# Performance work log

Measured on AMD Instinct MI355X. Metric: run time of the kernel, lower is better.

Reference implementation:

```python
import jax, jax.numpy as jnp
import numpy as np

POS_SCALE = 50.0
LEN_SCALE = 500.0

N_NODES = 100000
N_EDGES = 600000
IN_DIM = 128
HID_DIM = 128


def setup_inputs() -> dict:
    key = jax.random.key(0)
    ks = jax.random.split(key, 12)
    x = jax.random.normal(ks[0], (N_NODES, IN_DIM), dtype=jnp.float32)
    positions = jax.random.randint(ks[1], (N_NODES,), 0, 50, dtype=jnp.int64)
    lengths = jax.random.randint(ks[2], (N_NODES,), 0, 500, dtype=jnp.int64)
    edge_index = jax.random.randint(ks[3], (2, N_EDGES), 0, N_NODES, dtype=jnp.int64)
    reranker_scores = jax.random.normal(ks[4], (N_NODES,), dtype=jnp.float32)
    s = 1.0 / np.sqrt(IN_DIM + 2)
    fp_w = jax.random.uniform(ks[5], (IN_DIM + 2, IN_DIM), minval=-s, maxval=s, dtype=jnp.float32)
    fp_b = jnp.zeros((IN_DIM,), jnp.float32)
    s2 = 1.0 / np.sqrt(IN_DIM)
    lin_l_w = jax.random.uniform(ks[6], (IN_DIM, HID_DIM), minval=-s2, maxval=s2, dtype=jnp.float32)
    lin_l_b = jnp.zeros((HID_DIM,), jnp.float32)
    lin_r_w = jax.random.uniform(ks[7], (IN_DIM, HID_DIM), minval=-s2, maxval=s2, dtype=jnp.float32)
    res_w = jax.random.uniform(ks[8], (IN_DIM, HID_DIM), minval=-s2, maxval=s2, dtype=jnp.float32)
    res_b = jnp.zeros((HID_DIM,), jnp.float32)
    s3 = 1.0 / np.sqrt(HID_DIM)
    sh_w = jax.random.uniform(ks[9], (HID_DIM, 1), minval=-s3, maxval=s3, dtype=jnp.float32)
    sh_b = jnp.zeros((1,), jnp.float32)
    alpha = jnp.asarray(0.65, jnp.float32)
    return {
        "x": x, "positions": positions, "lengths": lengths,
        "edge_index": edge_index, "reranker_scores": reranker_scores,
        "fp_w": fp_w, "fp_b": fp_b,
        "lin_l_w": lin_l_w, "lin_l_b": lin_l_b, "lin_r_w": lin_r_w,
        "res_w": res_w, "res_b": res_b,
        "sh_w": sh_w, "sh_b": sh_b, "alpha": alpha,
    }


def reference(x, positions, lengths, edge_index, reranker_scores,
              fp_w, fp_b, lin_l_w, lin_l_b, lin_r_w, res_w, res_b,
              sh_w, sh_b, alpha):
    n = x.shape[0]
    # position/length features
    pos_feat = positions[:, None].astype(x.dtype) / POS_SCALE
    len_feat = lengths[:, None].astype(x.dtype) / LEN_SCALE
    xf = jnp.concatenate([x, pos_feat, len_feat], axis=-1)  # [N, D+2]
    xf = xf @ fp_w + fp_b                                   # [N, D]
    h_in = xf @ res_w + res_b                               # residual proj [N, H]
    # SAGEConv with mean aggregation: out = lin_l(mean_{j->i} x_j) + lin_r(x_i)
    src, dst = edge_index[0], edge_index[1]
    msg_sum = jax.ops.segment_sum(xf[src], dst, num_segments=n)          # [N, D]
    cnt = jax.ops.segment_sum(jnp.ones((src.shape[0], 1), xf.dtype), dst, num_segments=n)
    agg = msg_sum / jnp.maximum(cnt, 1.0)
    h = jax.nn.relu(agg @ lin_l_w + lin_l_b + xf @ lin_r_w)  # [N, H]
    # dropout is identity in eval mode
    h = h + h_in
    gnn_scores = (h @ sh_w + sh_b)[:, 0]                     # [N]
    a = jax.nn.sigmoid(alpha)
    return a * reranker_scores + (1.0 - a) * gnn_scores
```

## Files before the change

kernel.cpp:

```cpp
#include <hip/hip_runtime.h>
#include <hip/hip_bf16.h>
#include <cstdint>

#define D 128
#define LDSPITCH 136
#define CAP 32

typedef __attribute__((ext_vector_type(4))) float f32x4;
typedef __attribute__((ext_vector_type(8))) short s16x8;

__device__ __forceinline__ unsigned short f2b(float f) {
    union { float f; uint32_t u; } v; v.f = f;
    uint32_t b = v.u + 0x7fffu + ((v.u >> 16) & 1u);
    return (unsigned short)(b >> 16);
}
__device__ __forceinline__ float b2f(unsigned short u) {
    union { uint32_t u; float f; } v; v.u = ((uint32_t)u) << 16; return v.f;
}

__global__ __launch_bounds__(256) void k_prep(
    const float* __restrict__ fp_w, const float* __restrict__ lin_l_w,
    const float* __restrict__ lin_r_w,
    unsigned short* __restrict__ Btf, unsigned short* __restrict__ Btl,
    unsigned short* __restrict__ Btr,
    const float* __restrict__ res_w, const float* __restrict__ res_b,
    const float* __restrict__ sh_w, const float* __restrict__ sh_b,
    const float* __restrict__ alpha, float* __restrict__ c1, float* __restrict__ scal,
    int* __restrict__ cursor, int N) {
    int bid = blockIdx.x, tid = threadIdx.x;
    if (bid < 192) {
        int m = bid >> 6;
        int i = (bid & 63) * 256 + tid;
        const float* src = (m == 0) ? fp_w : (m == 1) ? lin_l_w : lin_r_w;
        unsigned short* dst = (m == 0) ? Btf : (m == 1) ? Btl : Btr;
        int k = i >> 7, n = i & 127;
        dst[n * D + k] = f2b(src[k * D + n]);
    } else if (bid == 192) {
        if (tid < 128) {
            float s = 0.f;
            for (int j = 0; j < D; ++j) s += res_w[tid * D + j] * sh_w[j];
            c1[tid] = s;
            if (tid == 0) {
                float c0 = 0.f;
                for (int j = 0; j < D; ++j) c0 += res_b[j] * sh_w[j];
                c0 += sh_b[0];
                float a = 1.f / (1.f + expf(-alpha[0]));
                scal[0] = a; scal[1] = c0;
            }
        }
    } else {
        int i = ((bid - 193) * 256 + tid) * 4;
        if (i < N) {
            if (i + 3 < N) *(int4*)(cursor + i) = (int4){0, 0, 0, 0};
            else { for (int k = i; k < N; ++k) cursor[k] = 0; }
        }
    }
}

__global__ __launch_bounds__(256) void k_gemm1(
    const float* __restrict__ x, unsigned short* __restrict__ xb,
    const int* __restrict__ positions, const int* __restrict__ lengths,
    const unsigned short* __restrict__ Btf,
    const float* __restrict__ fp_w, const float* __restrict__ fp_b,
    const float* __restrict__ c1, float* __restrict__ d1, int N, int mb,
    const int* __restrict__ ei, int* __restrict__ cursor, int* __restrict__ srcs, int E) {
    if (blockIdx.x >= mb) {
        int e = (blockIdx.x - mb) * 256 + threadIdx.x;
        if (e < E) {
            int src = ei[e];
            int dst = ei[E + e];
            int pos = atomicAdd(&cursor[dst], 1);
            if (pos < CAP) srcs[dst * CAP + pos] = src;
        }
        return;
    }
    int lane = threadIdx.x & 63;
    int wv = threadIdx.x >> 6;
    int col = lane & 15, q = lane >> 4;
    int row0 = blockIdx.x * 64 + wv * 16;
    int arow = row0 + col; if (arow > N - 1) arow = N - 1;

    f32x4 acc[8];
#pragma unroll
    for (int nt = 0; nt < 8; ++nt) acc[nt] = (f32x4){0.f, 0.f, 0.f, 0.f};

#pragma unroll
    for (int ks = 0; ks < 4; ++ks) {
        const float* xp = x + (size_t)arow * D + ks * 32 + q * 8;
        float4 a0 = *(const float4*)xp;
        float4 a1 = *(const float4*)(xp + 4);
        s16x8 af;
        af[0] = (short)f2b(a0.x); af[1] = (short)f2b(a0.y);
        af[2] = (short)f2b(a0.z); af[3] = (short)f2b(a0.w);
        af[4] = (short)f2b(a1.x); af[5] = (short)f2b(a1.y);
        af[6] = (short)f2b(a1.z); af[7] = (short)f2b(a1.w);
#pragma unroll
        for (int nt = 0; nt < 8; ++nt) {
            s16x8 bf = *(const s16x8*)(Btf + (size_t)(nt * 16 + col) * D + ks * 32 + q * 8);
            acc[nt] = __builtin_amdgcn_mfma_f32_16x16x32_bf16(af, bf, acc[nt], 0, 0, 0);
        }
    }

    float pf[4], lf[4];
#pragma unroll
    for (int r = 0; r < 4; ++r) {
        int rr = row0 + q * 4 + r; int rc = rr < N ? rr : N - 1;
        pf[r] = (float)positions[rc] * (1.0f / 50.0f);
        lf[r] = (float)lengths[rc] * (1.0f / 500.0f);
    }
    float sdot[4] = {0.f, 0.f, 0.f, 0.f};
#pragma unroll
    for (int nt = 0; nt < 8; ++nt) {
        int n = nt * 16 + col;
        float bias = fp_b[n];
        float w128 = fp_w[128 * D + n];
        float w129 = fp_w[129 * D + n];
        float c1v = c1[n];
#pragma unroll
        for (int r = 0; r < 4; ++r) {
            float t = acc[nt][r] + bias + pf[r] * w128 + lf[r] * w129;
            int rr = row0 + q * 4 + r;
            if (rr < N) xb[(size_t)rr * D + n] = f2b(t);
            sdot[r] += t * c1v;
        }
    }
#pragma unroll
    for (int r = 0; r < 4; ++r) {
        float s = sdot[r];
        s += __shfl_xor(s, 1, 64);
        s += __shfl_xor(s, 2, 64);
        s += __shfl_xor(s, 4, 64);
        s += __shfl_xor(s, 8, 64);
        if (col == 0) {
            int rr = row0 + q * 4 + r;
            if (rr < N) d1[rr] = s;
        }
    }
}

__global__ __launch_bounds__(256) void k_gemm2(
    const unsigned short* __restrict__ xfb,
    const int* __restrict__ cursor, const int* __restrict__ srcs,
    const unsigned short* __restrict__ Btl, const unsigned short* __restrict__ Btr,
    const float* __restrict__ lin_l_b, const float* __restrict__ sh_w,
    const float* __restrict__ rer, const float* __restrict__ d1,
    const float* __restrict__ scal, float* __restrict__ out, int N) {
    __shared__ unsigned short agg[64 * LDSPITCH];
    int lane = threadIdx.x & 63;
    int wv = threadIdx.x >> 6;
    int li = lane & 15, q = lane >> 4;
    int wrow0 = blockIdx.x * 64 + wv * 16;

#pragma unroll
    for (int rr = 0; rr < 4; ++rr) {
        int row = wrow0 + rr * 4 + q;
        float t[8] = {0.f, 0.f, 0.f, 0.f, 0.f, 0.f, 0.f, 0.f};
        int deg = 0;
        if (row < N) {
            deg = cursor[row]; if (deg > CAP) deg = CAP;
            const int* sp = srcs + (size_t)row * CAP;
            int dm1 = deg - 1;
            for (int j = 0; j < deg; j += 8) {
                int4 ia = *(const int4*)(sp + (j     < dm1 ? j     : (dm1 & ~3)));
                int4 ib;
                {
                    int jb = j + 4 <= dm1 ? j + 4 : (dm1 & ~3);
                    ib = *(const int4*)(sp + jb);
                }
                int idx[8];
                idx[0] = sp[j];
                idx[1] = j + 1 <= dm1 ? ia.y : sp[dm1];
                idx[2] = j + 2 <= dm1 ? ia.z : sp[dm1];
                idx[3] = j + 3 <= dm1 ? ia.w : sp[dm1];
                idx[4] = j + 4 <= dm1 ? ib.x : sp[dm1];
                idx[5] = j + 5 <= dm1 ? ib.y : sp[dm1];
                idx[6] = j + 6 <= dm1 ? ib.z : sp[dm1];
                idx[7] = j + 7 <= dm1 ? ib.w : sp[dm1];
                s16x8 v[8];
#pragma unroll
                for (int k = 0; k < 8; ++k)
                    v[k] = *(const s16x8*)(xfb + (size_t)idx[k] * D + li * 8);
                float w[8];
#pragma unroll
                for (int k = 0; k < 8; ++k) w[k] = (j + k < deg) ? 1.f : 0.f;
#pragma unroll
                for (int k = 0; k < 8; ++k)
#pragma unroll
                    for (int k2 = 0; k2 < 8; ++k2)
                        t[k2] += w[k] * b2f((unsigned short)v[k][k2]);
            }
        }
        float rc = 1.0f / (float)(deg > 0 ? deg : 1);
        s16x8 o;
#pragma unroll
        for (int k2 = 0; k2 < 8; ++k2) o[k2] = (short)f2b(t[k2] * rc);
        *(s16x8*)(agg + (wv * 16 + rr * 4 + q) * LDSPITCH + li * 8) = o;
    }

    int arow = wrow0 + li; if (arow > N - 1) arow = N - 1;

    f32x4 acc[8];
#pragma unroll
    for (int nt = 0; nt < 8; ++nt) acc[nt] = (f32x4){0.f, 0.f, 0.f, 0.f};

#pragma unroll
    for (int ks = 0; ks < 4; ++ks) {
        s16x8 af = *(const s16x8*)(agg + (wv * 16 + li) * LDSPITCH + ks * 32 + q * 8);
#pragma unroll
        for (int nt = 0; nt < 8; ++nt) {
            s16x8 bf = *(const s16x8*)(Btl + (size_t)(nt * 16 + li) * D + ks * 32 + q * 8);
            acc[nt] = __builtin_amdgcn_mfma_f32_16x16x32_bf16(af, bf, acc[nt], 0, 0, 0);
        }
    }
#pragma unroll
    for (int ks = 0; ks < 4; ++ks) {
        s16x8 af = *(const s16x8*)(xfb + (size_t)arow * D + ks * 32 + q * 8);
#pragma unroll
        for (int nt = 0; nt < 8; ++nt) {
            s16x8 bf = *(const s16x8*)(Btr + (size_t)(nt * 16 + li) * D + ks * 32 + q * 8);
            acc[nt] = __builtin_amdgcn_mfma_f32_16x16x32_bf16(af, bf, acc[nt], 0, 0, 0);
        }
    }

    float a = scal[0], c0 = scal[1];
    float sdot[4] = {0.f, 0.f, 0.f, 0.f};
#pragma unroll
    for (int nt = 0; nt < 8; ++nt) {
        int n = nt * 16 + li;
        float bias = lin_l_b[n];
        float shw = sh_w[n];
#pragma unroll
        for (int r = 0; r < 4; ++r) {
            float t = acc[nt][r] + bias;
            sdot[r] += fmaxf(t, 0.f) * shw;
        }
    }
#pragma unroll
    for (int r = 0; r < 4; ++r) {
        float s = sdot[r];
        s += __shfl_xor(s, 1, 64);
        s += __shfl_xor(s, 2, 64);
        s += __shfl_xor(s, 4, 64);
        s += __shfl_xor(s, 8, 64);
        if (li == 0) {
            int rr = wrow0 + q * 4 + r;
            if (rr < N) out[rr] = a * rer[rr] + (1.f - a) * (c0 + d1[rr] + s);
        }
    }
}

extern "C" void kernel_launch(void* const* d_in, const int* in_sizes, int n_in,
                              void* d_out, int out_size, void* d_ws, size_t ws_size,
                              hipStream_t stream) {
    const float* x        = (const float*)d_in[0];
    const int*   positions= (const int*)d_in[1];
    const int*   lengths  = (const int*)d_in[2];
    const int*   ei       = (const int*)d_in[3];
    const float* rer      = (const float*)d_in[4];
    const float* fp_w     = (const float*)d_in[5];
    const float* fp_b     = (const float*)d_in[6];
    const float* lin_l_w  = (const float*)d_in[7];
    const float* lin_l_b  = (const float*)d_in[8];
    const float* lin_r_w  = (const float*)d_in[9];
    const float* res_w    = (const float*)d_in[10];
    const float* res_b    = (const float*)d_in[11];
    const float* sh_w     = (const float*)d_in[12];
    const float* sh_b     = (const float*)d_in[13];
    const float* alpha    = (const float*)d_in[14];
    int N = in_sizes[1];
    int E = in_sizes[3] / 2;
    float* out = (float*)d_out;

    char* ws = (char*)d_ws;
    size_t off = 0;
    auto alloc = [&](size_t bytes) -> void* {
        void* p = ws + off;
        off = (off + bytes + 255) & ~(size_t)255;
        return p;
    };
    unsigned short* xb  = (unsigned short*)alloc((size_t)N * D * 2);
    int* srcs    = (int*)alloc((size_t)N * CAP * 4);
    int* cursor  = (int*)alloc((size_t)N * 4);
    float* d1    = (float*)alloc((size_t)N * 4);
    unsigned short* Btf = (unsigned short*)alloc(D * D * 2);
    unsigned short* Btl = (unsigned short*)alloc(D * D * 2);
    unsigned short* Btr = (unsigned short*)alloc(D * D * 2);
    float* c1    = (float*)alloc(D * 4);
    float* scal  = (float*)alloc(16);

    int mb = (N + 63) / 64;
    int cb = (E + 255) / 256;
    int zb = (N + 1023) / 1024;

    k_prep<<<193 + zb, 256, 0, stream>>>(fp_w, lin_l_w, lin_r_w, Btf, Btl, Btr,
                                         res_w, res_b, sh_w, sh_b, alpha, c1, scal,
                                         cursor, N);
    k_gemm1<<<mb + cb, 256, 0, stream>>>(x, xb, positions, lengths, Btf, fp_w, fp_b,
                                         c1, d1, N, mb, ei, cursor, srcs, E);
    k_gemm2<<<mb, 256, 0, stream>>>(xb, cursor, srcs, Btl, Btr, lin_l_b, sh_w, rer, d1, scal, out, N);
}
```

Baseline: 244.7 us.

## Batch first-chunk neighbor gathers across four rows to raise memory-level parallelism

Restructures the gather stage of the second GEMM kernel so that the neighbor-index vectors, degrees and the self-row A fragments for all four rows are loaded up front. The first eight neighbors of every row are then gathered unconditionally with clamped indices, and only rows with degree above eight fall into a tail loop. The aim is to issue many independent global loads at once to hide gather latency. It also interleaves the lin_l and lin_r MFMA passes with B fragments preloaded per k-step. The cost is higher register pressure, plus wasted loads of padding slots for low-degree rows, which rely on clamping to stay in bounds.

```diff
diff --git a/kernel.cpp b/kernel.cpp
--- a/kernel.cpp
+++ b/kernel.cpp
@@ -150,76 +150,118 @@
     int wv = threadIdx.x >> 6;
     int li = lane & 15, q = lane >> 4;
     int wrow0 = blockIdx.x * 64 + wv * 16;
-
+    int Nm1 = N - 1;
+
+    int rowc[4];
 #pragma unroll
     for (int rr = 0; rr < 4; ++rr) {
         int row = wrow0 + rr * 4 + q;
-        float t[8] = {0.f, 0.f, 0.f, 0.f, 0.f, 0.f, 0.f, 0.f};
-        int deg = 0;
-        if (row < N) {
-            deg = cursor[row]; if (deg > CAP) deg = CAP;
-            const int* sp = srcs + (size_t)row * CAP;
-            int dm1 = deg - 1;
-            for (int j = 0; j < deg; j += 8) {
-                int4 ia = *(const int4*)(sp + (j     < dm1 ? j     : (dm1 & ~3)));
-                int4 ib;
-                {
-                    int jb = j + 4 <= dm1 ? j + 4 : (dm1 & ~3);
-                    ib = *(const int4*)(sp + jb);
+        rowc[rr] = row < Nm1 ? row : Nm1;
+    }
+    int4 ia[4], ib[4];
+    int deg[4];
+#pragma unroll
+    for (int rr = 0; rr < 4; ++rr) {
+        const int* sp = srcs + (size_t)rowc[rr] * CAP;
+        ia[rr] = *(const int4*)sp;
+        ib[rr] = *(const int4*)(sp + 4);
+        deg[rr] = cursor[rowc[rr]];
+    }
+    int arow = wrow0 + li; if (arow > Nm1) arow = Nm1;
+    s16x8 afx[4];
+#pragma unroll
+    for (int ks = 0; ks < 4; ++ks)
+        afx[ks] = *(const s16x8*)(xfb + (size_t)arow * D + ks * 32 + q * 8);
+
+    float t[4][8];
+#pragma unroll
+    for (int rr = 0; rr < 4; ++rr)
+#pragma unroll
+        for (int k2 = 0; k2 < 8; ++k2) t[rr][k2] = 0.f;
+
+#pragma unroll
+    for (int rr = 0; rr < 4; ++rr) {
+        int dg = deg[rr] > CAP ? CAP : deg[rr];
+        int ix[8] = {ia[rr].x, ia[rr].y, ia[rr].z, ia[rr].w,
+                     ib[rr].x, ib[rr].y, ib[rr].z, ib[rr].w};
+        s16x8 v[8];
+#pragma unroll
+        for (int k = 0; k < 8; ++k) {
+            int c = ix[k];
+            c = c > 0 ? c : 0;
+            c = c < Nm1 ? c : Nm1;
+            v[k] = *(const s16x8*)(xfb + (size_t)c * D + li * 8);
+        }
+        float w[8];
+#pragma unroll
+        for (int k = 0; k < 8; ++k) w[k] = (k < dg) ? 1.f : 0.f;
+#pragma unroll
+        for (int k = 0; k < 8; ++k)
+#pragma unroll
+            for (int k2 = 0; k2 < 8; ++k2)
+                t[rr][k2] += w[k] * b2f((unsigned short)v[k][k2]);
+    }
+
+#pragma unroll
+    for (int rr = 0; rr < 4; ++rr) {
+        int dg = deg[rr] > CAP ? CAP : deg[rr];
+        if (dg > 8) {
+            const int* sp = srcs + (size_t)rowc[rr] * CAP;
+            for (int j = 8; j < dg; j += 8) {
+                int4 ic = *(const int4*)(sp + j);
+                int4 id = *(const int4*)(sp + j + 4);
+                int ix[8] = {ic.x, ic.y, ic.z, ic.w, id.x, id.y, id.z, id.w};
+                s16x8 v[8];
+#pragma unroll
+                for (int k = 0; k < 8; ++k) {
+                    int c = ix[k];
+                    c = c > 0 ? c : 0;
+                    c = c < Nm1 ? c : Nm1;
+                    v[k] = *(const s16x8*)(xfb + (size_t)c * D + li * 8);
                 }
-                int idx[8];
-                idx[0] = sp[j];
-                idx[1] = j + 1 <= dm1 ? ia.y : sp[dm1];
-                idx[2] = j + 2 <= dm1 ? ia.z : sp[dm1];
-                idx[3] = j + 3 <= dm1 ? ia.w : sp[dm1];
-                idx[4] = j + 4 <= dm1 ? ib.x : sp[dm1];
-                idx[5] = j + 5 <= dm1 ? ib.y : sp[dm1];
-                idx[6] = j + 6 <= dm1 ? ib.z : sp[dm1];
-                idx[7] = j + 7 <= dm1 ? ib.w : sp[dm1];
-                s16x8 v[8];
+                float w[8];
+#pragma unroll
+                for (int k = 0; k < 8; ++k) w[k] = (j + k < dg) ? 1.f : 0.f;
 #pragma unroll
                 for (int k = 0; k < 8; ++k)
-                    v[k] = *(const s16x8*)(xfb + (size_t)idx[k] * D + li * 8);
-                float w[8];
-#pragma unroll
-                for (int k = 0; k < 8; ++k) w[k] = (j + k < deg) ? 1.f : 0.f;
-#pragma unroll
-                for (int k = 0; k < 8; ++k)
 #pragma unroll
                     for (int k2 = 0; k2 < 8; ++k2)
-                        t[k2] += w[k] * b2f((unsigned short)v[k][k2]);
+                        t[rr][k2] += w[k] * b2f((unsigned short)v[k][k2]);
             }
         }
-        float rc = 1.0f / (float)(deg > 0 ? deg : 1);
+    }
+
+#pragma unroll
+    for (int rr = 0; rr < 4; ++rr) {
+        int dg = deg[rr] > CAP ? CAP : deg[rr];
+        float rc = 1.0f / (float)(dg > 0 ? dg : 1);
         s16x8 o;
 #pragma unroll
-        for (int k2 = 0; k2 < 8; ++k2) o[k2] = (short)f2b(t[k2] * rc);
+        for (int k2 = 0; k2 < 8; ++k2) o[k2] = (short)f2b(t[rr][k2] * rc);
         *(s16x8*)(agg + (wv * 16 + rr * 4 + q) * LDSPITCH + li * 8) = o;
     }
 
-    int arow = wrow0 + li; if (arow > N - 1) arow = N - 1;
-
     f32x4 acc[8];
 #pragma unroll
     for (int nt = 0; nt < 8; ++nt) acc[nt] = (f32x4){0.f, 0.f, 0.f, 0.f};
 
 #pragma unroll
     for (int ks = 0; ks < 4; ++ks) {
-        s16x8 af = *(const s16x8*)(agg + (wv * 16 + li) * LDSPITCH + ks * 32 + q * 8);
-#pragma unroll
-        for (int nt = 0; nt < 8; ++nt) {
-            s16x8 bf = *(const s16x8*)(Btl + (size_t)(nt * 16 + li) * D + ks * 32 + q * 8);
-            acc[nt] = __builtin_amdgcn_mfma_f32_16x16x32_bf16(af, bf, acc[nt], 0, 0, 0);
-        }
-    }
-#pragma unroll
-    for (int ks = 0; ks < 4; ++ks) {
-        s16x8 af = *(const s16x8*)(xfb + (size_t)arow * D + ks * 32 + q * 8);
-#pragma unroll
-        for (int nt = 0; nt < 8; ++nt) {
-            s16x8 bf = *(const s16x8*)(Btr + (size_t)(nt * 16 + li) * D + ks * 32 + q * 8);
-            acc[nt] = __builtin_amdgcn_mfma_f32_16x16x32_bf16(af, bf, acc[nt], 0, 0, 0);
-        }
+        s16x8 afa = *(const s16x8*)(agg + (wv * 16 + li) * LDSPITCH + ks * 32 + q * 8);
+        s16x8 bfl[8];
+#pragma unroll
+        for (int nt = 0; nt < 8; ++nt)
+            bfl[nt] = *(const s16x8*)(Btl + (size_t)(nt * 16 + li) * D + ks * 32 + q * 8);
+#pragma unroll
+        for (int nt = 0; nt < 8; ++nt)
+            acc[nt] = __builtin_amdgcn_mfma_f32_16x16x32_bf16(afa, bfl[nt], acc[nt], 0, 0, 0);
+        s16x8 bfr[8];
+#pragma unroll
+        for (int nt = 0; nt < 8; ++nt)
+            bfr[nt] = *(const s16x8*)(Btr + (size_t)(nt * 16 + li) * D + ks * 32 + q * 8);
+#pragma unroll
+        for (int nt = 0; nt < 8; ++nt)
+            acc[nt] = __builtin_amdgcn_mfma_f32_16x16x32_bf16(afx[ks], bfr[nt], acc[nt], 0, 0, 0);
     }
 
     float a = scal[0], c0 = scal[1];
@@ -231,8 +273,8 @@
         float shw = sh_w[n];
 #pragma unroll
         for (int r = 0; r < 4; ++r) {
-            float t = acc[nt][r] + bias;
-            sdot[r] += fmaxf(t, 0.f) * shw;
+            float tt = acc[nt][r] + bias;
+            sdot[r] += fmaxf(tt, 0.f) * shw;
         }
     }
 #pragma unroll
```

Result: slower. 250.7 us (+2.4%).
